# Performance work log

Measured on AMD Instinct MI355X. Metric: run time of the kernel, lower is better.

The kernel has to match this reference:

```python
import jax, jax.numpy as jnp
import numpy as np

B, S, H, NH, MAXW = 4, 512, 768, 4, 8
N = S * MAXW          # num_spans = seq_len * max_span_width
WD = 64               # width embedding dim
INNER = 3072          # ffn_ratio(4) * hidden? -> projection inner dim
IN_DIM = H + WD + H   # span_rep + width_emb + cls_rep = 1600


def setup_inputs() -> dict:
    key = jax.random.key(0)
    ks = jax.random.split(key, 16)
    token_reps = jax.random.normal(ks[0], (B, S, H), jnp.float32)
    starts = jax.random.randint(ks[1], (B, N), 0, S - MAXW)
    widths = jax.random.randint(ks[2], (B, N), 1, MAXW + 1)
    span_ids = jnp.stack([starts, starts + widths], axis=-1)  # [B,N,2], end exclusive
    span_masks = jax.random.bernoulli(ks[3], 0.9, (B, N))
    span_widths = widths  # indices into width table of size MAXW+1
    cls_reps = jax.random.normal(ks[4], (B, H), jnp.float32)
    # learned params
    cls_embedding = jax.random.normal(ks[5], (H,), jnp.float32) * 0.1
    in_proj_w = jax.random.normal(ks[6], (3 * H, H), jnp.float32) * 0.02
    in_proj_b = jnp.zeros((3 * H,), jnp.float32)
    out_proj_w = jax.random.normal(ks[7], (H, H), jnp.float32) * 0.02
    out_proj_b = jnp.zeros((H,), jnp.float32)
    width_table = jax.random.normal(ks[8], (MAXW + 1, WD), jnp.float32) * 0.02
    w1 = jax.random.normal(ks[9], (INNER, IN_DIM), jnp.float32) * 0.02
    b1 = jnp.zeros((INNER,), jnp.float32)
    w2 = jax.random.normal(ks[10], (H, INNER), jnp.float32) * 0.02
    b2 = jnp.zeros((H,), jnp.float32)
    return dict(token_reps=token_reps, span_ids=span_ids, span_masks=span_masks,
                cls_reps=cls_reps, span_widths=span_widths,
                cls_embedding=cls_embedding, in_proj_w=in_proj_w, in_proj_b=in_proj_b,
                out_proj_w=out_proj_w, out_proj_b=out_proj_b, width_table=width_table,
                w1=w1, b1=b1, w2=w2, b2=b2)


def _forward(token_reps, cls_reps, cls_embedding, in_proj_w, in_proj_b,
             out_proj_w, out_proj_b, width_table, w1, b1, w2, b2,
             span_ids, span_masks, span_widths):
    b, s, h = token_reps.shape
    n = span_ids.shape[1]
    dh = h // NH
    # per-span content masks over the (cls + tokens) axis -> [B,N,S+1], True = valid key
    starts = span_ids[..., 0]
    ends = span_ids[..., 1] - 1
    rng = jnp.arange(s)[None, None, :]
    content = (rng >= starts[..., None]) & (rng <= ends[..., None]) & span_masks[..., None]
    mask = jnp.concatenate([jnp.ones((b, n, 1), bool), content], axis=-1)
    # sequence with prepended CLS; K/V are identical across spans, compute once per batch
    x = jnp.concatenate([jnp.broadcast_to(cls_embedding, (b, 1, h)), token_reps], axis=1)
    wq, wk, wv = jnp.split(in_proj_w, 3, axis=0)
    bq, bk, bv = jnp.split(in_proj_b, 3, axis=0)
    # only the CLS query row of the MHA output is kept downstream, so compute it alone
    q = (cls_embedding @ wq.T + bq).reshape(NH, dh)          # [H] -> [NH,dh]
    kh = (x @ wk.T + bk).reshape(b, s + 1, NH, dh)
    vh = (x @ wv.T + bv).reshape(b, s + 1, NH, dh)
    scale = 1.0 / jnp.sqrt(jnp.asarray(dh, token_reps.dtype))
    base_scores = jnp.einsum('hd,bshd->bhs', q, kh) * scale   # [B,NH,S+1], shared by spans
    neg = jnp.asarray(-1e30, base_scores.dtype)
    scores = jnp.where(mask[:, :, None, :], base_scores[:, None, :, :], neg)  # [B,N,NH,S+1]
    attn = jax.nn.softmax(scores, axis=-1)
    ctx = jnp.einsum('bnhs,bshd->bnhd', attn, vh).reshape(b, n, h)
    span_reps = ctx @ out_proj_w.T + out_proj_b               # [B,N,H]
    width_emb = width_table[span_widths]                       # [B,N,WD]
    cls_exp = jnp.broadcast_to(cls_reps[:, None, :], (b, n, h))
    feats = jnp.concatenate([span_reps, width_emb, cls_exp], axis=-1)  # [B,N,1600]
    h1 = jax.nn.relu(feats @ w1.T + b1)
    return h1 @ w2.T + b2                                      # [B,N,H]


def reference(token_reps, span_ids, span_masks, cls_reps, span_widths,
              cls_embedding, in_proj_w, in_proj_b, out_proj_w, out_proj_b,
              width_table, w1, b1, w2, b2):
    return _forward(token_reps, cls_reps, cls_embedding, in_proj_w, in_proj_b,
                    out_proj_w, out_proj_b, width_table, w1, b1, w2, b2,
                    span_ids, span_masks, span_widths)
```

## Files before the change

kernel.cpp:

```cpp
#include <hip/hip_runtime.h>
#include <hip/hip_bf16.h>
#include <math.h>

#define B_      4
#define S_      512
#define H_      768
#define NH_     4
#define DH_     192
#define N_      4096
#define WD_     64
#define INNER_  3072
#define INDIM_  1600
#define SP1     513
#define ROWS_X  (B_*SP1)
#define ROWS_XP 2176
#define NSPAN   (B_*N_)
#define KEYS_PB 41472
#define KEYSPACE (4*KEYS_PB)
#define MUPADMAX 16640

typedef __attribute__((ext_vector_type(8))) short bf16x8;
typedef __attribute__((ext_vector_type(4))) float f32x4;

__device__ __forceinline__ unsigned short f2bf(float f){
    unsigned u = __builtin_bit_cast(unsigned, f);
    u = u + 0x7FFFu + ((u >> 16) & 1u);
    return (unsigned short)(u >> 16);
}
__device__ __forceinline__ float bf2f(unsigned hs){
    return __builtin_bit_cast(float, hs << 16);
}

__device__ __forceinline__ float wave_sum(float p){
    #pragma unroll
    for (int off = 32; off > 0; off >>= 1) p += __shfl_down(p, off);
    return p;
}

__device__ __forceinline__ void gld16(unsigned short* lds, const unsigned short* g){
    __builtin_amdgcn_global_load_lds(
        (const __attribute__((address_space(1))) unsigned int*)(const void*)g,
        (__attribute__((address_space(3))) unsigned int*)(void*)lds,
        16, 0, 0);
}

__device__ __forceinline__ void wgbar(){
    asm volatile("" ::: "memory");
    __builtin_amdgcn_s_barrier();
    asm volatile("" ::: "memory");
}
#define VMW(n) asm volatile("s_waitcnt vmcnt(" #n ")" ::: "memory")

__global__ __launch_bounds__(256) void mega_prep(
    const float* __restrict__ token_reps, const float* __restrict__ cls_emb,
    const float* __restrict__ in_proj_w, const float* __restrict__ in_proj_b,
    const float* __restrict__ out_proj_w, const float* __restrict__ out_proj_b,
    const float* __restrict__ cls_reps, const float* __restrict__ wtab,
    const float* __restrict__ w1, const float* __restrict__ b1,
    const float* __restrict__ w2, const unsigned* __restrict__ masks,
    unsigned short* __restrict__ Xb, unsigned short* __restrict__ Wv,
    unsigned short* __restrict__ W2b, unsigned short* __restrict__ W1a,
    unsigned short* __restrict__ OutT, float* __restrict__ qbuf,
    float* __restrict__ BiasC, float* __restrict__ WC, int* __restrict__ flag)
{
    int b = blockIdx.x, t = threadIdx.x;
    __shared__ float tile[32][33];
    __shared__ int s_any;
    int wave = t >> 6, lane = t & 63;

    if (b < 576){
        long i = (long)b * 256 + t;
        float4 v = ((const float4*)(in_proj_w + (size_t)1536 * H_))[i];
        ushort4 o; o.x = f2bf(v.x); o.y = f2bf(v.y); o.z = f2bf(v.z); o.w = f2bf(v.w);
        ((ushort4*)Wv)[i] = o;
    } else if ((b -= 576) < 2304){
        long i = (long)b * 256 + t;
        float4 v = ((const float4*)w2)[i];
        ushort4 o; o.x = f2bf(v.x); o.y = f2bf(v.y); o.z = f2bf(v.z); o.w = f2bf(v.w);
        ((ushort4*)W2b)[i] = o;
    } else if ((b -= 2304) < 2052){
        int r = b;
        int bb = r / SP1, s = r % SP1;
        const float* src = (s == 0) ? cls_emb : &token_reps[((long)bb * S_ + (s - 1)) * H_];
        for (int d = t; d < H_; d += 256)
            Xb[(long)r * H_ + d] = f2bf(src[d]);
    } else if ((b -= 2052) < 3072){
        if (t < 192){
            float4 v = ((const float4*)&w1[(long)b * INDIM_])[t];
            ushort4 o; o.x = f2bf(v.x); o.y = f2bf(v.y); o.z = f2bf(v.z); o.w = f2bf(v.w);
            ((ushort4*)&W1a[(long)b * 768])[t] = o;
        }
    } else if ((b -= 3072) < 576){
        int bx = (b % 24) * 32, by = (b / 24) * 32;
        int tx = t & 31, ty = t >> 5;
        #pragma unroll
        for (int r = 0; r < 32; r += 8)
            tile[ty + r][tx] = out_proj_w[(long)(by + ty + r) * 768 + bx + tx];
        __syncthreads();
        #pragma unroll
        for (int r = 0; r < 32; r += 8)
            OutT[(long)(bx + ty + r) * 768 + by + tx] = f2bf(tile[tx][ty + r]);
    } else if ((b -= 576) < 192){
        int j = b * 4 + wave;
        const float* wr = &in_proj_w[(long)j * H_];
        float p = 0.f;
        #pragma unroll
        for (int i = 0; i < 12; ++i) p += cls_emb[lane + 64*i] * wr[lane + 64*i];
        p = wave_sum(p);
        if (lane == 0) qbuf[j] = p + in_proj_b[j];
    } else if ((b -= 192) < 768){
        int i = b * 4 + wave;
        const float* row = &w1[(long)i * INDIM_];
        float p0 = 0.f, pb0 = 0.f, pb1 = 0.f, pb2 = 0.f, pb3 = 0.f;
        #pragma unroll
        for (int k0 = 0; k0 < 12; ++k0){
            int k = lane + 64*k0;
            p0 += out_proj_b[k] * row[k];
            float rv = row[832 + k];
            pb0 += cls_reps[0*H_ + k] * rv;
            pb1 += cls_reps[1*H_ + k] * rv;
            pb2 += cls_reps[2*H_ + k] * rv;
            pb3 += cls_reps[3*H_ + k] * rv;
        }
        p0 = wave_sum(p0); pb0 = wave_sum(pb0); pb1 = wave_sum(pb1);
        pb2 = wave_sum(pb2); pb3 = wave_sum(pb3);
        if (lane == 0){
            float base = b1[i] + p0;
            BiasC[0*INNER_ + i] = base + pb0;
            BiasC[1*INNER_ + i] = base + pb1;
            BiasC[2*INNER_ + i] = base + pb2;
            BiasC[3*INNER_ + i] = base + pb3;
        }
    } else if ((b -= 768) < 768){
        int i = b * 4 + wave;
        float rv = w1[(long)i * INDIM_ + 768 + lane];
        #pragma unroll
        for (int w = 0; w < 9; ++w){
            float p = wave_sum(wtab[w * WD_ + lane] * rv);
            if (lane == 0) WC[w * INNER_ + i] = p;
        }
    } else {
        if (t == 0) s_any = 0;
        __syncthreads();
        int any = 0;
        for (int i = t; i < 4096; i += 256){
            unsigned v = masks[i];
            if (!(v == 0u || v == 1u || v == 0x3F800000u)) any = 1;
        }
        if (any) s_any = 1;
        __syncthreads();
        if (t == 0) *flag = s_any;
    }
}

__global__ __launch_bounds__(256) void u_mark(
    const float* __restrict__ q, const float* __restrict__ in_proj_w,
    const float* __restrict__ in_proj_b, float* __restrict__ u,
    const int* __restrict__ span_ids, const void* __restrict__ masks,
    const int* __restrict__ flag, const int* __restrict__ span_widths,
    int* __restrict__ keyarr, unsigned char* __restrict__ present)
{
    int blk = blockIdx.x, t = threadIdx.x;
    if (blk < 12){
        int idx = blk * 256 + t;
        int h = idx / 768, k = idx % 768;
        float s = 0.f;
        for (int j = 0; j < 192; ++j)
            s += q[h*192 + j] * in_proj_w[(long)(768 + h*192 + j) * 768 + k];
        u[idx] = s;
        if (idx < 4){
            float c = 0.f;
            for (int j = 0; j < 192; ++j) c += q[idx*192 + j] * in_proj_b[768 + idx*192 + j];
            u[3072 + idx] = c;
        }
    } else {
        int span = (blk - 12) * 256 + t;
        int start = span_ids[span*2], end = span_ids[span*2+1];
        bool sm = (*flag == 0) ? (((const unsigned*)masks)[span] != 0u)
                               : (((const unsigned char*)masks)[span] != 0);
        int cnt = sm ? (end - start) : 0;
        if (cnt < 0) cnt = 0;
        if (cnt > 8) cnt = 8;
        if (start < 0) start = 0;
        if (start > 511) start = 511;
        if (start + cnt > S_) cnt = S_ - start;
        if (cnt == 0) start = 0;
        int w = span_widths[span];
        w = (w < 0) ? 0 : ((w > 8) ? 8 : w);
        int b = span >> 12;
        int key = b * KEYS_PB + (start * 9 + cnt) * 9 + w;
        keyarr[span] = key;
        present[key] = 1;
    }
}

__global__ __launch_bounds__(256) void scores2(
    const float* __restrict__ token_reps, const float* __restrict__ cls_emb,
    const float* __restrict__ u, float* __restrict__ SC)
{
    int r = blockIdx.x;
    int b = r / SP1, s = r % SP1;
    const float* src = (s == 0) ? cls_emb : &token_reps[((long)b * S_ + (s - 1)) * H_];
    int h = threadIdx.x >> 6, lane = threadIdx.x & 63;
    float p = 0.f;
    #pragma unroll
    for (int i = 0; i < 12; ++i) p += src[lane + 64*i] * u[h*768 + lane + 64*i];
    p = wave_sum(p);
    if (lane == 0){
        const float scale = 0.0721687836487032f;
        SC[((long)(b * NH_ + h)) * SP1 + s] = (p + u[3072 + h]) * scale;
    }
}

__global__ __launch_bounds__(256) void scanB(const unsigned* __restrict__ present4,
                                             int* __restrict__ blockCnt){
    __shared__ int sh[256];
    int blk = blockIdx.x, t = threadIdx.x;
    unsigned w = present4[blk*256 + t];
    int c = (w & 1) + ((w >> 8) & 1) + ((w >> 16) & 1) + ((w >> 24) & 1);
    sh[t] = c; __syncthreads();
    for (int off = 128; off > 0; off >>= 1){
        if (t < off) sh[t] += sh[t + off];
        __syncthreads();
    }
    if (t == 0) blockCnt[blk] = sh[0];
}

__global__ __launch_bounds__(256) void scanC(const int* __restrict__ blockCnt,
                                             int* __restrict__ blockOff, int* __restrict__ mu){
    __shared__ int sh[256];
    int t = threadIdx.x;
    int v = (t < 162) ? blockCnt[t] : 0;
    sh[t] = v; __syncthreads();
    for (int off = 1; off < 256; off <<= 1){
        int add = (t >= off) ? sh[t - off] : 0;
        __syncthreads();
        sh[t] += add;
        __syncthreads();
    }
    if (t < 162) blockOff[t] = sh[t] - v;
    if (t == 161){ mu[0] = sh[161]; mu[1] = (sh[161] + 255) & ~255; }
}

__global__ __launch_bounds__(256) void scanD(const unsigned* __restrict__ present4,
                                             const int* __restrict__ blockOff,
                                             int* __restrict__ slotOf, int* __restrict__ slotPack,
                                             int* __restrict__ widthsU){
    __shared__ int sh[256];
    int blk = blockIdx.x, t = threadIdx.x;
    unsigned w = present4[blk*256 + t];
    int c = (w & 1) + ((w >> 8) & 1) + ((w >> 16) & 1) + ((w >> 24) & 1);
    sh[t] = c; __syncthreads();
    for (int off = 1; off < 256; off <<= 1){
        int add = (t >= off) ? sh[t - off] : 0;
        __syncthreads();
        sh[t] += add;
        __syncthreads();
    }
    int slot = blockOff[blk] + sh[t] - c;
    #pragma unroll
    for (int i = 0; i < 4; ++i){
        if ((w >> (8*i)) & 1){
            int k = blk*1024 + t*4 + i;
            slotOf[k] = slot;
            int b = k / KEYS_PB, kl = k % KEYS_PB;
            int width = kl % 9, sc2 = kl / 9;
            int cnt = sc2 % 9, start = sc2 / 9;
            slotPack[slot] = start | (cnt << 9) | (width << 13) | (b << 17);
            widthsU[slot]  = width | (b << 4);
            slot++;
        }
    }
}

__global__ __launch_bounds__(192) void attn_spanmap(
    const int* __restrict__ mu, const int* __restrict__ slotPack,
    const float* __restrict__ SC, const unsigned short* __restrict__ VB,
    unsigned short* __restrict__ CTXU,
    const int* __restrict__ keyarr, const int* __restrict__ slotOf,
    int* __restrict__ slotspan)
{
    int blk = blockIdx.x, t = threadIdx.x;
    if (blk >= MUPADMAX){
        int s = (blk - MUPADMAX) * 192 + t;
        if (s < NSPAN) slotspan[s] = slotOf[keyarr[s]];
        return;
    }
    int slot = blk;
    if (slot >= mu[0]) return;
    int pk = slotPack[slot];
    int start = pk & 511, cnt = (pk >> 9) & 15, b = (pk >> 17) & 3;
    __shared__ float w_sh[NH_][12];

    if (t < NH_){
        int h = t;
        const float* sc = &SC[((long)(b * NH_ + h)) * SP1];
        float m = sc[0];
        for (int j = 0; j < cnt; ++j) m = fmaxf(m, sc[1 + start + j]);
        float e0 = expf(sc[0] - m), sum = e0;
        float ej[8];
        for (int j = 0; j < cnt; ++j){ ej[j] = expf(sc[1 + start + j] - m); sum += ej[j]; }
        float inv = 1.f / sum;
        w_sh[h][0] = e0 * inv;
        for (int j = 0; j < cnt; ++j) w_sh[h][1 + j] = ej[j] * inv;
    }
    __syncthreads();

    long ctxbase = (long)slot * H_;
    const unsigned short* V0 = VB + (long)(b * SP1) * 768;
    #pragma unroll
    for (int i = 0; i < 2; ++i){
        int p = t + 192 * i;
        int d = p * 2;
        int h = d / DH_;
        float w0 = w_sh[h][0];
        unsigned v = ((const unsigned*)V0)[p];
        float a0 = w0 * bf2f(v & 0xffffu), a1 = w0 * bf2f(v >> 16);
        for (int j = 0; j < cnt; ++j){
            unsigned vv = *(const unsigned*)(V0 + (long)(1 + start + j) * 768 + d);
            float wj = w_sh[h][1 + j];
            a0 += wj * bf2f(vv & 0xffffu);
            a1 += wj * bf2f(vv >> 16);
        }
        ((unsigned*)(CTXU + ctxbase))[p] = (unsigned)f2bf(a0) | ((unsigned)f2bf(a1) << 16);
    }
}

__global__ __launch_bounds__(256) void gather_out2(
    const int* __restrict__ slotspan, const float* __restrict__ OutU,
    const unsigned short* __restrict__ P1, const float* __restrict__ b2,
    float* __restrict__ out)
{
    const long total = (long)NSPAN * 192;
    long stride = (long)gridDim.x * 256;
    for (long idx = (long)blockIdx.x * 256 + threadIdx.x; idx < total; idx += stride){
        long s = idx / 192, d = idx % 192;
        long so = (long)slotspan[s] * 192 + d;
        float4 a = ((const float4*)OutU)[so];
        ushort4 p = ((const ushort4*)P1)[so];
        float4 bb = ((const float4*)b2)[d];
        float4 o;
        o.x = a.x + bf2f(p.x) + bb.x;
        o.y = a.y + bf2f(p.y) + bb.y;
        o.z = a.z + bf2f(p.z) + bb.z;
        o.w = a.w + bf2f(p.w) + bb.w;
        ((float4*)out)[idx] = o;
    }
}

template<int EPI>
__global__ __launch_bounds__(256, 2) void gemm97(
    const unsigned short* __restrict__ A, const unsigned short* __restrict__ Bm,
    const float* __restrict__ biasA, void* __restrict__ Cp,
    int M, int N, int K, int lda, int ldb, int ldc, int nbx)
{
    __shared__ unsigned short As[128 * 32];
    __shared__ unsigned short Bs[128 * 32];
    const int t = threadIdx.x, lane = t & 63, wave = t >> 6;
    const int wr = wave >> 1, wcid = wave & 1;

    int nwg = gridDim.x;
    int bid = blockIdx.x;
    int swz = ((nwg & 7) == 0) ? ((bid & 7) * (nwg >> 3) + (bid >> 3)) : bid;
    const int m0 = (swz / nbx) * 128;
    const int n0 = (swz % nbx) * 128;

    f32x4 acc[4][4];
    #pragma unroll
    for (int i = 0; i < 4; ++i)
        #pragma unroll
        for (int j = 0; j < 4; ++j)
            acc[i][j] = (f32x4){0.f, 0.f, 0.f, 0.f};

    const unsigned short* gA = A + (long)(m0 + wave*32 + (lane >> 2)) * lda + (lane & 3) * 8;
    const unsigned short* gB = Bm + (long)(n0 + wave*32 + (lane >> 2)) * ldb + (lane & 3) * 8;
    unsigned short* lA = &As[wave * 32 * 32];
    unsigned short* lB = &Bs[wave * 32 * 32];
    const long a16 = (long)16 * lda, b16 = (long)16 * ldb;

    for (int k0 = 0; k0 < K; k0 += 32){
        gld16(lA,       gA + k0);
        gld16(lA + 512, gA + a16 + k0);
        gld16(lB,       gB + k0);
        gld16(lB + 512, gB + b16 + k0);
        __syncthreads();

        bf16x8 af[4], bfr[4];
        #pragma unroll
        for (int f = 0; f < 4; ++f){
            af[f]  = *(const bf16x8*)&As[(wr*64 + f*16 + (lane & 15)) * 32 + (lane >> 4) * 8];
            bfr[f] = *(const bf16x8*)&Bs[(wcid*64 + f*16 + (lane & 15)) * 32 + (lane >> 4) * 8];
        }
        #pragma unroll
        for (int i = 0; i < 4; ++i)
            #pragma unroll
            for (int j = 0; j < 4; ++j)
                acc[i][j] = __builtin_amdgcn_mfma_f32_16x16x32_bf16(af[i], bfr[j], acc[i][j], 0, 0, 0);
        __syncthreads();
    }

    const int r0 = (lane >> 4) * 4;
    const int cc = lane & 15;
    #pragma unroll
    for (int i = 0; i < 4; ++i){
        int rowb = m0 + wr*64 + i*16 + r0;
        #pragma unroll
        for (int j = 0; j < 4; ++j){
            int col = n0 + wcid*64 + j*16 + cc;
            float cb = biasA ? biasA[col] : 0.f;
            #pragma unroll
            for (int r = 0; r < 4; ++r){
                long o = (long)(rowb + r) * ldc + col;
                float v = acc[i][j][r] + cb;
                if (EPI == 1) ((unsigned short*)Cp)[o] = f2bf(v);
                else          ((float*)Cp)[o] = v;
            }
        }
    }
}

template<int EPI, int LDA_, int LDB_>
__global__ __launch_bounds__(512, 2) void gemm256v4(
    const unsigned short* __restrict__ A, const unsigned short* __restrict__ Bm,
    const float* __restrict__ biasA, const float* __restrict__ biasB,
    const int* __restrict__ widths, void* __restrict__ Cp,
    int K, int ldc, int nbx, const int* __restrict__ mu,
    unsigned short* __restrict__ Cp1)
{
    __shared__ __align__(16) unsigned char lds[131072];
    const int t = threadIdx.x, lane = t & 63;
    const int wave = t >> 6;
    const int wr = wave >> 2, wc = wave & 3;

    int nwg = gridDim.x, bid = blockIdx.x;
    int sp = 0;
    if (EPI == 3){
        int nh = nwg >> 1;
        sp = (bid >= nh) ? 1 : 0;
        bid -= sp * nh;
        nwg = nh;
    }
    int swz = ((nwg & 7) == 0) ? ((bid & 7) * (nwg >> 3) + (bid >> 3)) : bid;
    const int m0 = (swz / nbx) * 256;
    const int n0 = (swz % nbx) * 256;
    if (mu && m0 >= mu[1]) return;

    const int Keff = (EPI == 3) ? (K >> 1) : K;
    const unsigned short* Ab = A + (EPI == 3 ? (long)sp * Keff : 0);
    const unsigned short* Bb = Bm + (EPI == 3 ? (long)sp * Keff : 0);

    const int rQ = t >> 3;
    const int cswz = ((t & 7) ^ (rQ & 7)) << 3;
    const unsigned short* sA = Ab + (long)(m0 + rQ) * LDA_ + cswz;
    const unsigned short* sB = Bb + (long)(n0 + ((rQ >> 5) * 64 + (rQ & 31))) * LDB_ + cswz;
    const int wsl = wave * 1024;

    const int aRow = (wr * 64 + (lane & 15)) * 128;
    const int bRow = (wc * 32 + (lane & 15)) * 128;
    const int pcl0 = (((lane >> 4) * 16)) ^ ((lane & 7) << 4);
    const int pcl1 = (64 + ((lane >> 4) * 16)) ^ ((lane & 7) << 4);

    f32x4 acc[8][4];
    #pragma unroll
    for (int i = 0; i < 8; ++i)
        #pragma unroll
        for (int j = 0; j < 4; ++j)
            acc[i][j] = (f32x4){0.f, 0.f, 0.f, 0.f};

    const int KT = Keff >> 6;
    bf16x8 aL[4][2], aH[4][2], bE[2][2], bO[2][2];

#define STG_(off, src) gld16((unsigned short*)(void*)(lds + (off) + wsl), (src))
#define RD_AL(fi, base) { aL[fi][0] = *(const bf16x8*)(lds + (base) + aRow + (fi)*2048 + pcl0); \
                          aL[fi][1] = *(const bf16x8*)(lds + (base) + aRow + (fi)*2048 + pcl1); }
#define RD_AH(fi, base) { aH[fi][0] = *(const bf16x8*)(lds + (base) + 16384 + aRow + (fi)*2048 + pcl0); \
                          aH[fi][1] = *(const bf16x8*)(lds + (base) + 16384 + aRow + (fi)*2048 + pcl1); }
#define RD_BE(jj, base) { bE[jj][0] = *(const bf16x8*)(lds + (base) + (jj)*2048 + bRow + pcl0); \
                          bE[jj][1] = *(const bf16x8*)(lds + (base) + (jj)*2048 + bRow + pcl1); }
#define RD_BO(jj, base) { bO[jj][0] = *(const bf16x8*)(lds + (base) + 16384 + (jj)*2048 + bRow + pcl0); \
                          bO[jj][1] = *(const bf16x8*)(lds + (base) + 16384 + (jj)*2048 + bRow + pcl1); }
#define Q_MFMA(AR, BR, I0, J0) \
    __builtin_amdgcn_s_setprio(1); \
    _Pragma("unroll") \
    for (int i = 0; i < 4; ++i) \
        _Pragma("unroll") \
        for (int j = 0; j < 2; ++j){ \
            acc[(I0)+i][(J0)+j] = __builtin_amdgcn_mfma_f32_16x16x32_bf16(AR[i][0], BR[j][0], acc[(I0)+i][(J0)+j], 0, 0, 0); \
            acc[(I0)+i][(J0)+j] = __builtin_amdgcn_mfma_f32_16x16x32_bf16(AR[i][1], BR[j][1], acc[(I0)+i][(J0)+j], 0, 0, 0); \
        } \
    __builtin_amdgcn_s_setprio(0);

    STG_(0,             sA);
    STG_(8192,          sA + 128 * LDA_);
    STG_(65536,         sB);
    STG_(65536 + 8192,  sB + 128 * LDB_);
    STG_(65536 + 16384, sB + 32 * LDB_);
    STG_(65536 + 24576, sB + 160 * LDB_);
    STG_(16384,         sA + 64 * LDA_);
    STG_(24576,         sA + 192 * LDA_);
    VMW(4);
    wgbar();
    RD_AL(0, 0u); RD_AL(1, 0u);
    RD_BE(0, 65536u); RD_BE(1, 65536u);

    for (int kt = 0; kt < KT - 1; ++kt){
        const unsigned rA = (unsigned)(kt & 1) * 32768u;
        const unsigned rB = 65536u + rA;
        const unsigned wA = rA ^ 32768u;
        const unsigned wB = 65536u + wA;
        const unsigned short* pA = sA + (long)(kt + 1) * 64;
        const unsigned short* pB = sB + (long)(kt + 1) * 64;

        VMW(2);
        STG_(wA, pA); STG_(wA + 8192, pA + 128 * LDA_);
        wgbar();
        RD_AL(2, rA); RD_AL(3, rA);
        RD_BO(0, rB); RD_BO(1, rB);
        Q_MFMA(aL, bE, 0, 0);

        VMW(2);
        STG_(wB, pB); STG_(wB + 8192, pB + 128 * LDB_);
        wgbar();
        RD_AH(0, rA); RD_AH(1, rA);
        Q_MFMA(aL, bO, 0, 2);

        STG_(wB + 16384, pB + 32 * LDB_); STG_(wB + 24576, pB + 160 * LDB_);
        wgbar();
        RD_AH(2, rA); RD_AH(3, rA);
        Q_MFMA(aH, bE, 4, 0);

        VMW(2);
        STG_(wA + 16384, pA + 64 * LDA_); STG_(wA + 24576, pA + 192 * LDA_);
        wgbar();
        RD_AL(0, wA); RD_AL(1, wA);
        RD_BE(0, wB); RD_BE(1, wB);
        Q_MFMA(aH, bO, 4, 2);
    }

    {
        const unsigned rA = (unsigned)((KT - 1) & 1) * 32768u;
        const unsigned rB = 65536u + rA;
        VMW(2);
        wgbar();
        RD_AL(2, rA); RD_AL(3, rA);
        RD_BO(0, rB); RD_BO(1, rB);
        Q_MFMA(aL, bE, 0, 0);
        VMW(0);
        wgbar();
        RD_AH(0, rA); RD_AH(1, rA);
        Q_MFMA(aL, bO, 0, 2);
        RD_AH(2, rA); RD_AH(3, rA);
        Q_MFMA(aH, bE, 4, 0);
        Q_MFMA(aH, bO, 4, 2);
    }
#undef STG_
#undef RD_AL
#undef RD_AH
#undef RD_BE
#undef RD_BO
#undef Q_MFMA

    const int r0 = (lane >> 4) * 4;
    const int cc = lane & 15;
    const int Nn = nbx * 256;

    if (EPI == 2){
        wgbar();
        #pragma unroll
        for (int mq = 0; mq < 2; ++mq){
            #pragma unroll
            for (int i = 0; i < 4; ++i){
                #pragma unroll
                for (int r = 0; r < 4; ++r){
                    int row = wr*128 + mq*64 + i*16 + r0 + r;
                    int wb = widths[m0 + row];
                    int wv = wb & 15, bb = (wb >> 4) & 3;
                    const float* bcl = biasA + (long)bb * Nn;
                    const float* wcb = biasB + (long)wv * Nn;
                    unsigned key = (unsigned)((row & 7) << 4);
                    unsigned rbase = (unsigned)row * 512u;
                    #pragma unroll
                    for (int j = 0; j < 4; ++j){
                        int col = wc*64 + j*16 + cc;
                        float v = acc[4*mq + i][j][r] + bcl[n0 + col] + wcb[n0 + col];
                        v = fmaxf(v, 0.f);
                        *(unsigned short*)(lds + rbase + (((unsigned)col * 2u) ^ key)) = f2bf(v);
                    }
                }
            }
        }
        wgbar();
        #pragma unroll
        for (int k = 0; k < 16; ++k){
            int row = (t >> 5) + k*16;
            int l32 = t & 31;
            bf16x8 val = *(const bf16x8*)(lds + (unsigned)row*512u
                             + (((unsigned)l32*16u) ^ ((unsigned)(row & 7) << 4)));
            *(bf16x8*)((unsigned short*)Cp + (long)(m0 + row) * ldc + n0 + l32*8) = val;
        }
    } else if (EPI == 3 && sp == 1){
        wgbar();
        #pragma unroll
        for (int mq = 0; mq < 2; ++mq){
            #pragma unroll
            for (int i = 0; i < 4; ++i){
                #pragma unroll
                for (int r = 0; r < 4; ++r){
                    int row = wr*128 + mq*64 + i*16 + r0 + r;
                    unsigned key = (unsigned)((row & 7) << 4);
                    unsigned rbase = (unsigned)row * 512u;
                    #pragma unroll
                    for (int j = 0; j < 4; ++j){
                        int col = wc*64 + j*16 + cc;
                        *(unsigned short*)(lds + rbase + (((unsigned)col * 2u) ^ key))
                            = f2bf(acc[4*mq + i][j][r]);
                    }
                }
            }
        }
        wgbar();
        #pragma unroll
        for (int k = 0; k < 16; ++k){
            int row = (t >> 5) + k*16;
            int l32 = t & 31;
            bf16x8 val = *(const bf16x8*)(lds + (unsigned)row*512u
                             + (((unsigned)l32*16u) ^ ((unsigned)(row & 7) << 4)));
            *(bf16x8*)(Cp1 + (long)(m0 + row) * ldc + n0 + l32*8) = val;
        }
    } else {
        #pragma unroll
        for (int h = 0; h < 2; ++h){
            wgbar();
            if (wr == h){
                #pragma unroll
                for (int mq = 0; mq < 2; ++mq){
                    #pragma unroll
                    for (int i = 0; i < 4; ++i){
                        #pragma unroll
                        for (int r = 0; r < 4; ++r){
                            int rloc = mq*64 + i*16 + r0 + r;
                            unsigned key = (unsigned)((rloc & 7) << 4);
                            unsigned rbase = (unsigned)rloc * 1024u;
                            #pragma unroll
                            for (int j = 0; j < 4; ++j){
                                int col = wc*64 + j*16 + cc;
                                float v = acc[4*mq + i][j][r] + (biasA ? biasA[n0 + col] : 0.f);
                                *(float*)(lds + rbase + (((unsigned)col * 4u) ^ key)) = v;
                            }
                        }
                    }
                }
            }
            wgbar();
            #pragma unroll
            for (int k = 0; k < 16; ++k){
                int rloc = (t >> 6) + k*8;
                int l64 = t & 63;
                f32x4 val = *(const f32x4*)(lds + (unsigned)rloc*1024u
                                 + (((unsigned)l64*16u) ^ ((unsigned)(rloc & 7) << 4)));
                *(f32x4*)((float*)Cp + (long)(m0 + 128*h + rloc) * ldc + n0 + l64*4) = val;
            }
        }
    }
}

extern "C" void kernel_launch(void* const* d_in, const int* in_sizes, int n_in,
                              void* d_out, int out_size, void* d_ws, size_t ws_size,
                              hipStream_t stream)
{
    const float* token_reps  = (const float*)d_in[0];
    const int*   span_ids    = (const int*)d_in[1];
    const void*  span_masks  = d_in[2];
    const float* cls_reps    = (const float*)d_in[3];
    const int*   span_widths = (const int*)d_in[4];
    const float* cls_emb     = (const float*)d_in[5];
    const float* in_proj_w   = (const float*)d_in[6];
    const float* in_proj_b   = (const float*)d_in[7];
    const float* out_proj_w  = (const float*)d_in[8];
    const float* out_proj_b  = (const float*)d_in[9];
    const float* width_table = (const float*)d_in[10];
    const float* w1          = (const float*)d_in[11];
    const float* b1          = (const float*)d_in[12];
    const float* w2          = (const float*)d_in[13];
    const float* b2          = (const float*)d_in[14];

    char* ws = (char*)d_ws;
    size_t off = 0;
    auto alloc = [&](size_t bytes)->char*{
        char* p = ws + off;
        off += (bytes + 255) & ~(size_t)255;
        return p;
    };
    int*            flag    = (int*)           alloc(4);
    float*          qbuf    = (float*)         alloc((size_t)H_ * 4);
    float*          ubuf    = (float*)         alloc((size_t)(3072 + 4) * 4);
    unsigned short* Xb      = (unsigned short*)alloc((size_t)ROWS_XP * H_ * 2);
    unsigned short* Wv      = (unsigned short*)alloc((size_t)H_ * H_ * 2);
    unsigned short* VB      = (unsigned short*)alloc((size_t)ROWS_XP * H_ * 2);
    float*          SC      = (float*)         alloc((size_t)B_ * NH_ * SP1 * 4);
    int*            keyarr  = (int*)           alloc((size_t)NSPAN * 4);
    unsigned char*  present = (unsigned char*) alloc((size_t)KEYSPACE);
    int*            blockCnt= (int*)           alloc((size_t)162 * 4);
    int*            blockOff= (int*)           alloc((size_t)162 * 4);
    int*            slotOf  = (int*)           alloc((size_t)KEYSPACE * 4);
    int*            slotPack= (int*)           alloc((size_t)MUPADMAX * 4);
    int*            widthsU = (int*)           alloc((size_t)MUPADMAX * 4);
    int*            slotspan= (int*)           alloc((size_t)NSPAN * 4);
    int*            mu      = (int*)           alloc(8);
    unsigned short* CTXU    = (unsigned short*)alloc((size_t)MUPADMAX * H_ * 2);
    unsigned short* W1a     = (unsigned short*)alloc((size_t)INNER_ * H_ * 2);
    unsigned short* OutT    = (unsigned short*)alloc((size_t)H_ * H_ * 2);
    unsigned short* Wfuse   = (unsigned short*)alloc((size_t)INNER_ * H_ * 2);
    unsigned short* W2b     = (unsigned short*)alloc((size_t)H_ * INNER_ * 2);
    unsigned short* H1U     = (unsigned short*)alloc((size_t)MUPADMAX * INNER_ * 2);
    float*          OutU    = (float*)         alloc((size_t)MUPADMAX * H_ * 4);
    float*          BiasC   = (float*)         alloc((size_t)B_ * INNER_ * 4);
    float*          WC      = (float*)         alloc((size_t)9 * INNER_ * 4);
    unsigned short* P1      = CTXU;
    (void)ws_size; (void)in_sizes; (void)n_in; (void)out_size;

    hipMemsetAsync(present, 0, KEYSPACE, stream);
    hipMemsetAsync(widthsU, 0, (size_t)MUPADMAX * 4, stream);

    mega_prep<<<576 + 2304 + 2052 + 3072 + 576 + 192 + 768 + 768 + 1, 256, 0, stream>>>(
        token_reps, cls_emb, in_proj_w, in_proj_b, out_proj_w, out_proj_b,
        cls_reps, width_table, w1, b1, w2, (const unsigned*)span_masks,
        Xb, Wv, W2b, W1a, OutT, qbuf, BiasC, WC, flag);

    u_mark<<<76, 256, 0, stream>>>(qbuf, in_proj_w, in_proj_b, ubuf,
                                   span_ids, span_masks, flag, span_widths,
                                   keyarr, present);

    gemm97<1><<<(768/128) * (INNER_/128), 256, 0, stream>>>(
        W1a, OutT, nullptr, Wfuse, INNER_, 768, 768, 768, 768, 768, 768/128);

    gemm97<1><<<(768/128) * (ROWS_XP/128), 256, 0, stream>>>(
        Xb, Wv, in_proj_b + 1536, VB, ROWS_XP, 768, 768, 768, 768, 768, 768/128);

    scores2<<<ROWS_X, 256, 0, stream>>>(token_reps, cls_emb, ubuf, SC);

    scanB<<<162, 256, 0, stream>>>((const unsigned*)present, blockCnt);
    scanC<<<1, 256, 0, stream>>>(blockCnt, blockOff, mu);
    scanD<<<162, 256, 0, stream>>>((const unsigned*)present, blockOff,
                                   slotOf, slotPack, widthsU);

    attn_spanmap<<<MUPADMAX + 86, 192, 0, stream>>>(
        mu, slotPack, SC, VB, CTXU, keyarr, slotOf, slotspan);

    gemm256v4<2, 768, 768><<<(MUPADMAX/256) * (INNER_/256), 512, 0, stream>>>(
        CTXU, Wfuse, BiasC, WC, widthsU, H1U, 768, INNER_, INNER_/256, mu, nullptr);

    gemm256v4<3, 3072, 3072><<<2 * (MUPADMAX/256) * (768/256), 512, 0, stream>>>(
        H1U, W2b, nullptr, nullptr, nullptr, OutU, 3072, 768, 768/256, mu, P1);

    gather_out2<<<2048, 256, 0, stream>>>(slotspan, OutU, P1, b2, (float*)d_out);
}
```

Before: 248.6 us.

## Merge mid-stage kernels, drop memsets and scanC, store split-K partials as bf16

Folds the two 128-tile GEMMs and the score kernel into one launch (mid_kernel). The zeroing of the present bitmap moves into extra mega_prep blocks, and the memset of widthsU is removed. scanC is merged into scanD, with each block redoing the small prefix over block counts. The first split-K partial of the second FFN GEMM is now written as bf16 instead of fp32, and the XCD swizzle is generalised to grid sizes that are not multiples of 8. The aim is fewer launches and less memory traffic. In exchange, the first partial loses precision and padded widthsU entries are no longer explicitly zeroed.

```diff
diff --git a/kernel.cpp b/kernel.cpp
--- a/kernel.cpp
+++ b/kernel.cpp
@@ -61,7 +61,8 @@
     unsigned short* __restrict__ Xb, unsigned short* __restrict__ Wv,
     unsigned short* __restrict__ W2b, unsigned short* __restrict__ W1a,
     unsigned short* __restrict__ OutT, float* __restrict__ qbuf,
-    float* __restrict__ BiasC, float* __restrict__ WC, int* __restrict__ flag)
+    float* __restrict__ BiasC, float* __restrict__ WC, int* __restrict__ flag,
+    unsigned* __restrict__ presentW)
 {
     int b = blockIdx.x, t = threadIdx.x;
     __shared__ float tile[32][33];
@@ -139,7 +140,7 @@
             float p = wave_sum(wtab[w * WD_ + lane] * rv);
             if (lane == 0) WC[w * INNER_ + i] = p;
         }
-    } else {
+    } else if ((b -= 768) < 1){
         if (t == 0) s_any = 0;
         __syncthreads();
         int any = 0;
@@ -150,6 +151,9 @@
         if (any) s_any = 1;
         __syncthreads();
         if (t == 0) *flag = s_any;
+    } else {
+        b -= 1;
+        presentW[b * 256 + t] = 0u;
     }
 }
 
@@ -194,21 +198,105 @@
     }
 }
 
-__global__ __launch_bounds__(256) void scores2(
+template<int EPI>
+__device__ __forceinline__ void gemm97_body(
+    int bid, int nwg,
+    const unsigned short* __restrict__ A, const unsigned short* __restrict__ Bm,
+    const float* __restrict__ biasA, void* __restrict__ Cp,
+    int M, int N, int K, int lda, int ldb, int ldc, int nbx,
+    unsigned short* As, unsigned short* Bs)
+{
+    const int t = threadIdx.x, lane = t & 63, wave = t >> 6;
+    const int wr = wave >> 1, wcid = wave & 1;
+
+    int swz = ((nwg & 7) == 0) ? ((bid & 7) * (nwg >> 3) + (bid >> 3)) : bid;
+    const int m0 = (swz / nbx) * 128;
+    const int n0 = (swz % nbx) * 128;
+
+    f32x4 acc[4][4];
+    #pragma unroll
+    for (int i = 0; i < 4; ++i)
+        #pragma unroll
+        for (int j = 0; j < 4; ++j)
+            acc[i][j] = (f32x4){0.f, 0.f, 0.f, 0.f};
+
+    const unsigned short* gA = A + (long)(m0 + wave*32 + (lane >> 2)) * lda + (lane & 3) * 8;
+    const unsigned short* gB = Bm + (long)(n0 + wave*32 + (lane >> 2)) * ldb + (lane & 3) * 8;
+    unsigned short* lA = &As[wave * 32 * 32];
+    unsigned short* lB = &Bs[wave * 32 * 32];
+    const long a16 = (long)16 * lda, b16 = (long)16 * ldb;
+
+    for (int k0 = 0; k0 < K; k0 += 32){
+        gld16(lA,       gA + k0);
+        gld16(lA + 512, gA + a16 + k0);
+        gld16(lB,       gB + k0);
+        gld16(lB + 512, gB + b16 + k0);
+        __syncthreads();
+
+        bf16x8 af[4], bfr[4];
+        #pragma unroll
+        for (int f = 0; f < 4; ++f){
+            af[f]  = *(const bf16x8*)&As[(wr*64 + f*16 + (lane & 15)) * 32 + (lane >> 4) * 8];
+            bfr[f] = *(const bf16x8*)&Bs[(wcid*64 + f*16 + (lane & 15)) * 32 + (lane >> 4) * 8];
+        }
+        #pragma unroll
+        for (int i = 0; i < 4; ++i)
+            #pragma unroll
+            for (int j = 0; j < 4; ++j)
+                acc[i][j] = __builtin_amdgcn_mfma_f32_16x16x32_bf16(af[i], bfr[j], acc[i][j], 0, 0, 0);
+        __syncthreads();
+    }
+
+    const int r0 = (lane >> 4) * 4;
+    const int cc = lane & 15;
+    #pragma unroll
+    for (int i = 0; i < 4; ++i){
+        int rowb = m0 + wr*64 + i*16 + r0;
+        #pragma unroll
+        for (int j = 0; j < 4; ++j){
+            int col = n0 + wcid*64 + j*16 + cc;
+            float cb = biasA ? biasA[col] : 0.f;
+            #pragma unroll
+            for (int r = 0; r < 4; ++r){
+                long o = (long)(rowb + r) * ldc + col;
+                float v = acc[i][j][r] + cb;
+                if (EPI == 1) ((unsigned short*)Cp)[o] = f2bf(v);
+                else          ((float*)Cp)[o] = v;
+            }
+        }
+    }
+}
+
+__global__ __launch_bounds__(256) void mid_kernel(
+    const unsigned short* __restrict__ W1a, const unsigned short* __restrict__ OutT,
+    unsigned short* __restrict__ Wfuse,
+    const unsigned short* __restrict__ Xb, const unsigned short* __restrict__ Wv,
+    const float* __restrict__ bv, unsigned short* __restrict__ VB,
     const float* __restrict__ token_reps, const float* __restrict__ cls_emb,
     const float* __restrict__ u, float* __restrict__ SC)
 {
-    int r = blockIdx.x;
-    int b = r / SP1, s = r % SP1;
-    const float* src = (s == 0) ? cls_emb : &token_reps[((long)b * S_ + (s - 1)) * H_];
-    int h = threadIdx.x >> 6, lane = threadIdx.x & 63;
-    float p = 0.f;
-    #pragma unroll
-    for (int i = 0; i < 12; ++i) p += src[lane + 64*i] * u[h*768 + lane + 64*i];
-    p = wave_sum(p);
-    if (lane == 0){
-        const float scale = 0.0721687836487032f;
-        SC[((long)(b * NH_ + h)) * SP1 + s] = (p + u[3072 + h]) * scale;
+    __shared__ unsigned short As[128 * 32];
+    __shared__ unsigned short Bs[128 * 32];
+    int blk = blockIdx.x;
+    if (blk < 144){
+        gemm97_body<1>(blk, 144, W1a, OutT, nullptr, Wfuse,
+                       INNER_, 768, 768, 768, 768, 768, 6, As, Bs);
+    } else if (blk < 246){
+        gemm97_body<1>(blk - 144, 102, Xb, Wv, bv, VB,
+                       ROWS_XP, 768, 768, 768, 768, 768, 6, As, Bs);
+    } else {
+        int r = blk - 246;
+        int b = r / SP1, s = r % SP1;
+        const float* src = (s == 0) ? cls_emb : &token_reps[((long)b * S_ + (s - 1)) * H_];
+        int h = threadIdx.x >> 6, lane = threadIdx.x & 63;
+        float p = 0.f;
+        #pragma unroll
+        for (int i = 0; i < 12; ++i) p += src[lane + 64*i] * u[h*768 + lane + 64*i];
+        p = wave_sum(p);
+        if (lane == 0){
+            const float scale = 0.0721687836487032f;
+            SC[((long)(b * NH_ + h)) * SP1 + s] = (p + u[3072 + h]) * scale;
+        }
     }
 }
 
@@ -226,28 +314,23 @@
     if (t == 0) blockCnt[blk] = sh[0];
 }
 
-__global__ __launch_bounds__(256) void scanC(const int* __restrict__ blockCnt,
-                                             int* __restrict__ blockOff, int* __restrict__ mu){
-    __shared__ int sh[256];
-    int t = threadIdx.x;
-    int v = (t < 162) ? blockCnt[t] : 0;
-    sh[t] = v; __syncthreads();
-    for (int off = 1; off < 256; off <<= 1){
-        int add = (t >= off) ? sh[t - off] : 0;
-        __syncthreads();
-        sh[t] += add;
-        __syncthreads();
-    }
-    if (t < 162) blockOff[t] = sh[t] - v;
-    if (t == 161){ mu[0] = sh[161]; mu[1] = (sh[161] + 255) & ~255; }
-}
-
 __global__ __launch_bounds__(256) void scanD(const unsigned* __restrict__ present4,
-                                             const int* __restrict__ blockOff,
+                                             const int* __restrict__ blockCnt,
                                              int* __restrict__ slotOf, int* __restrict__ slotPack,
-                                             int* __restrict__ widthsU){
+                                             int* __restrict__ widthsU, int* __restrict__ mu){
+    __shared__ int offs[256];
     __shared__ int sh[256];
     int blk = blockIdx.x, t = threadIdx.x;
+    int v = (t < 162) ? blockCnt[t] : 0;
+    offs[t] = v; __syncthreads();
+    for (int off = 1; off < 256; off <<= 1){
+        int add = (t >= off) ? offs[t - off] : 0;
+        __syncthreads();
+        offs[t] += add;
+        __syncthreads();
+    }
+    if (blk == 0 && t == 161){ mu[0] = offs[161]; mu[1] = (offs[161] + 255) & ~255; }
+    int blockBase = (blk == 0) ? 0 : offs[blk - 1];
     unsigned w = present4[blk*256 + t];
     int c = (w & 1) + ((w >> 8) & 1) + ((w >> 16) & 1) + ((w >> 24) & 1);
     sh[t] = c; __syncthreads();
@@ -257,7 +340,7 @@
         sh[t] += add;
         __syncthreads();
     }
-    int slot = blockOff[blk] + sh[t] - c;
+    int slot = blockBase + sh[t] - c;
     #pragma unroll
     for (int i = 0; i < 4; ++i){
         if ((w >> (8*i)) & 1){
@@ -326,8 +409,8 @@
     }
 }
 
-__global__ __launch_bounds__(256) void gather_out2(
-    const int* __restrict__ slotspan, const float* __restrict__ OutU,
+__global__ __launch_bounds__(256) void gather_out3(
+    const int* __restrict__ slotspan, const unsigned short* __restrict__ P0,
     const unsigned short* __restrict__ P1, const float* __restrict__ b2,
     float* __restrict__ out)
 {
@@ -336,86 +419,15 @@
     for (long idx = (long)blockIdx.x * 256 + threadIdx.x; idx < total; idx += stride){
         long s = idx / 192, d = idx % 192;
         long so = (long)slotspan[s] * 192 + d;
-        float4 a = ((const float4*)OutU)[so];
-        ushort4 p = ((const ushort4*)P1)[so];
+        ushort4 p0 = ((const ushort4*)P0)[so];
+        ushort4 p1 = ((const ushort4*)P1)[so];
         float4 bb = ((const float4*)b2)[d];
         float4 o;
-        o.x = a.x + bf2f(p.x) + bb.x;
-        o.y = a.y + bf2f(p.y) + bb.y;
-        o.z = a.z + bf2f(p.z) + bb.z;
-        o.w = a.w + bf2f(p.w) + bb.w;
+        o.x = bf2f(p0.x) + bf2f(p1.x) + bb.x;
+        o.y = bf2f(p0.y) + bf2f(p1.y) + bb.y;
+        o.z = bf2f(p0.z) + bf2f(p1.z) + bb.z;
+        o.w = bf2f(p0.w) + bf2f(p1.w) + bb.w;
         ((float4*)out)[idx] = o;
-    }
-}
-
-template<int EPI>
-__global__ __launch_bounds__(256, 2) void gemm97(
-    const unsigned short* __restrict__ A, const unsigned short* __restrict__ Bm,
-    const float* __restrict__ biasA, void* __restrict__ Cp,
-    int M, int N, int K, int lda, int ldb, int ldc, int nbx)
-{
-    __shared__ unsigned short As[128 * 32];
-    __shared__ unsigned short Bs[128 * 32];
-    const int t = threadIdx.x, lane = t & 63, wave = t >> 6;
-    const int wr = wave >> 1, wcid = wave & 1;
-
-    int nwg = gridDim.x;
-    int bid = blockIdx.x;
-    int swz = ((nwg & 7) == 0) ? ((bid & 7) * (nwg >> 3) + (bid >> 3)) : bid;
-    const int m0 = (swz / nbx) * 128;
-    const int n0 = (swz % nbx) * 128;
-
-    f32x4 acc[4][4];
-    #pragma unroll
-    for (int i = 0; i < 4; ++i)
-        #pragma unroll
-        for (int j = 0; j < 4; ++j)
-            acc[i][j] = (f32x4){0.f, 0.f, 0.f, 0.f};
-
-    const unsigned short* gA = A + (long)(m0 + wave*32 + (lane >> 2)) * lda + (lane & 3) * 8;
-    const unsigned short* gB = Bm + (long)(n0 + wave*32 + (lane >> 2)) * ldb + (lane & 3) * 8;
-    unsigned short* lA = &As[wave * 32 * 32];
-    unsigned short* lB = &Bs[wave * 32 * 32];
-    const long a16 = (long)16 * lda, b16 = (long)16 * ldb;
-
-    for (int k0 = 0; k0 < K; k0 += 32){
-        gld16(lA,       gA + k0);
-        gld16(lA + 512, gA + a16 + k0);
-        gld16(lB,       gB + k0);
-        gld16(lB + 512, gB + b16 + k0);
-        __syncthreads();
-
-        bf16x8 af[4], bfr[4];
-        #pragma unroll
-        for (int f = 0; f < 4; ++f){
-            af[f]  = *(const bf16x8*)&As[(wr*64 + f*16 + (lane & 15)) * 32 + (lane >> 4) * 8];
-            bfr[f] = *(const bf16x8*)&Bs[(wcid*64 + f*16 + (lane & 15)) * 32 + (lane >> 4) * 8];
-        }
-        #pragma unroll
-        for (int i = 0; i < 4; ++i)
-            #pragma unroll
-            for (int j = 0; j < 4; ++j)
-                acc[i][j] = __builtin_amdgcn_mfma_f32_16x16x32_bf16(af[i], bfr[j], acc[i][j], 0, 0, 0);
-        __syncthreads();
-    }
-
-    const int r0 = (lane >> 4) * 4;
-    const int cc = lane & 15;
-    #pragma unroll
-    for (int i = 0; i < 4; ++i){
-        int rowb = m0 + wr*64 + i*16 + r0;
-        #pragma unroll
-        for (int j = 0; j < 4; ++j){
-            int col = n0 + wcid*64 + j*16 + cc;
-            float cb = biasA ? biasA[col] : 0.f;
-            #pragma unroll
-            for (int r = 0; r < 4; ++r){
-                long o = (long)(rowb + r) * ldc + col;
-                float v = acc[i][j][r] + cb;
-                if (EPI == 1) ((unsigned short*)Cp)[o] = f2bf(v);
-                else          ((float*)Cp)[o] = v;
-            }
-        }
     }
 }
 
@@ -440,7 +452,9 @@
         bid -= sp * nh;
         nwg = nh;
     }
-    int swz = ((nwg & 7) == 0) ? ((bid & 7) * (nwg >> 3) + (bid >> 3)) : bid;
+    int q = nwg >> 3, rr = nwg & 7;
+    int xcd = bid & 7, idx8 = bid >> 3;
+    int swz = (xcd < rr ? xcd * (q + 1) : rr * (q + 1) + (xcd - rr) * q) + idx8;
     const int m0 = (swz / nbx) * 256;
     const int n0 = (swz % nbx) * 256;
     if (mu && m0 >= mu[1]) return;
@@ -598,7 +612,8 @@
                              + (((unsigned)l32*16u) ^ ((unsigned)(row & 7) << 4)));
             *(bf16x8*)((unsigned short*)Cp + (long)(m0 + row) * ldc + n0 + l32*8) = val;
         }
-    } else if (EPI == 3 && sp == 1){
+    } else if (EPI == 3){
+        unsigned short* dst = sp ? Cp1 : (unsigned short*)Cp;
         wgbar();
         #pragma unroll
         for (int mq = 0; mq < 2; ++mq){
@@ -625,7 +640,7 @@
             int l32 = t & 31;
             bf16x8 val = *(const bf16x8*)(lds + (unsigned)row*512u
                              + (((unsigned)l32*16u) ^ ((unsigned)(row & 7) << 4)));
-            *(bf16x8*)(Cp1 + (long)(m0 + row) * ldc + n0 + l32*8) = val;
+            *(bf16x8*)(dst + (long)(m0 + row) * ldc + n0 + l32*8) = val;
         }
     } else {
         #pragma unroll
@@ -701,7 +716,6 @@
     int*            keyarr  = (int*)           alloc((size_t)NSPAN * 4);
     unsigned char*  present = (unsigned char*) alloc((size_t)KEYSPACE);
     int*            blockCnt= (int*)           alloc((size_t)162 * 4);
-    int*            blockOff= (int*)           alloc((size_t)162 * 4);
     int*            slotOf  = (int*)           alloc((size_t)KEYSPACE * 4);
     int*            slotPack= (int*)           alloc((size_t)MUPADMAX * 4);
     int*            widthsU = (int*)           alloc((size_t)MUPADMAX * 4);
@@ -712,37 +726,29 @@
     unsigned short* OutT    = (unsigned short*)alloc((size_t)H_ * H_ * 2);
     unsigned short* Wfuse   = (unsigned short*)alloc((size_t)INNER_ * H_ * 2);
     unsigned short* W2b     = (unsigned short*)alloc((size_t)H_ * INNER_ * 2);
-    unsigned short* H1U     = (unsigned short*)alloc((size_t)MUPADMAX * INNER_ * 2);
-    float*          OutU    = (float*)         alloc((size_t)MUPADMAX * H_ * 4);
     float*          BiasC   = (float*)         alloc((size_t)B_ * INNER_ * 4);
     float*          WC      = (float*)         alloc((size_t)9 * INNER_ * 4);
+    unsigned short* H1U     = (unsigned short*)alloc((size_t)MUPADMAX * INNER_ * 2);
+    unsigned short* P0      = (unsigned short*)alloc((size_t)MUPADMAX * H_ * 2);
     unsigned short* P1      = CTXU;
     (void)ws_size; (void)in_sizes; (void)n_in; (void)out_size;
 
-    hipMemsetAsync(present, 0, KEYSPACE, stream);
-    hipMemsetAsync(widthsU, 0, (size_t)MUPADMAX * 4, stream);
-
-    mega_prep<<<576 + 2304 + 2052 + 3072 + 576 + 192 + 768 + 768 + 1, 256, 0, stream>>>(
+    mega_prep<<<576 + 2304 + 2052 + 3072 + 576 + 192 + 768 + 768 + 1 + 162, 256, 0, stream>>>(
         token_reps, cls_emb, in_proj_w, in_proj_b, out_proj_w, out_proj_b,
         cls_reps, width_table, w1, b1, w2, (const unsigned*)span_masks,
-        Xb, Wv, W2b, W1a, OutT, qbuf, BiasC, WC, flag);
+        Xb, Wv, W2b, W1a, OutT, qbuf, BiasC, WC, flag, (unsigned*)present);
 
     u_mark<<<76, 256, 0, stream>>>(qbuf, in_proj_w, in_proj_b, ubuf,
                                    span_ids, span_masks, flag, span_widths,
                                    keyarr, present);
 
-    gemm97<1><<<(768/128) * (INNER_/128), 256, 0, stream>>>(
-        W1a, OutT, nullptr, Wfuse, INNER_, 768, 768, 768, 768, 768, 768/128);
-
-    gemm97<1><<<(768/128) * (ROWS_XP/128), 256, 0, stream>>>(
-        Xb, Wv, in_proj_b + 1536, VB, ROWS_XP, 768, 768, 768, 768, 768, 768/128);
-
-    scores2<<<ROWS_X, 256, 0, stream>>>(token_reps, cls_emb, ubuf, SC);
+    mid_kernel<<<144 + 102 + 2052, 256, 0, stream>>>(
+        W1a, OutT, Wfuse, Xb, Wv, in_proj_b + 1536, VB,
+        token_reps, cls_emb, ubuf, SC);
 
     scanB<<<162, 256, 0, stream>>>((const unsigned*)present, blockCnt);
-    scanC<<<1, 256, 0, stream>>>(blockCnt, blockOff, mu);
-    scanD<<<162, 256, 0, stream>>>((const unsigned*)present, blockOff,
-                                   slotOf, slotPack, widthsU);
+    scanD<<<162, 256, 0, stream>>>((const unsigned*)present, blockCnt,
+                                   slotOf, slotPack, widthsU, mu);
 
     attn_spanmap<<<MUPADMAX + 86, 192, 0, stream>>>(
         mu, slotPack, SC, VB, CTXU, keyarr, slotOf, slotspan);
@@ -751,7 +757,7 @@
         CTXU, Wfuse, BiasC, WC, widthsU, H1U, 768, INNER_, INNER_/256, mu, nullptr);
 
     gemm256v4<3, 3072, 3072><<<2 * (MUPADMAX/256) * (768/256), 512, 0, stream>>>(
-        H1U, W2b, nullptr, nullptr, nullptr, OutU, 3072, 768, 768/256, mu, P1);
-
-    gather_out2<<<2048, 256, 0, stream>>>(slotspan, OutU, P1, b2, (float*)d_out);
-}
+        H1U, W2b, nullptr, nullptr, nullptr, P0, 3072, 768, 768/256, mu, P1);
+
+    gather_out3<<<2048, 256, 0, stream>>>(slotspan, P0, P1, b2, (float*)d_out);
+}
```

After: 289.0 us. +16.2%, slower.
